# Optimization experiments

Hardware: AMD Instinct MI355X
Metric: run time of the kernel (lower is better)

## Reference

```python
import jax, jax.numpy as jnp
import numpy as np

D_MODEL = 512
PROJ = 2 * D_MODEL  # 1024
N_STATES = 32
KSIZE = 4
LN_EPS = 1e-3  # keras LayerNormalization default epsilon


def setup_inputs() -> dict:
    key = jax.random.key(0)
    ks = jax.random.split(key, 16)
    B, L = 2, 2048
    s_in = 1.0 / np.sqrt(D_MODEL)
    s_pr = 1.0 / np.sqrt(PROJ)
    x = jax.random.normal(ks[0], (B, L, D_MODEL), dtype=jnp.float32)
    # LayerNorm params
    ln_gamma = jnp.ones((D_MODEL,), jnp.float32)
    ln_beta = jnp.zeros((D_MODEL,), jnp.float32)
    # dense1 / dense2: d_model -> proj
    W1 = jax.random.normal(ks[1], (D_MODEL, PROJ), jnp.float32) * s_in
    b1 = jnp.zeros((PROJ,), jnp.float32)
    W2 = jax.random.normal(ks[2], (D_MODEL, PROJ), jnp.float32) * s_in
    b2 = jnp.zeros((PROJ,), jnp.float32)
    # depthwise causal conv1d: kernel (K, 1, PROJ) in WIO layout, groups=PROJ
    conv_k = jax.random.normal(ks[3], (KSIZE, 1, PROJ), jnp.float32) * 0.5
    conv_b = jnp.zeros((PROJ,), jnp.float32)
    # SSM params
    A_log = jnp.log(jnp.broadcast_to(jnp.arange(1, N_STATES + 1, dtype=jnp.float32), (PROJ, N_STATES)))
    D_skip = jnp.ones((PROJ,), jnp.float32)
    WB = jax.random.normal(ks[4], (PROJ, N_STATES), jnp.float32) * s_pr
    bB = jnp.zeros((N_STATES,), jnp.float32)
    WC = jax.random.normal(ks[5], (PROJ, N_STATES), jnp.float32) * s_pr
    bC = jnp.zeros((N_STATES,), jnp.float32)
    Wd = jax.random.normal(ks[6], (PROJ, PROJ), jnp.float32) * s_pr
    bd = jnp.zeros((PROJ,), jnp.float32)
    # dense3: proj -> d_model
    W3 = jax.random.normal(ks[7], (PROJ, D_MODEL), jnp.float32) * s_pr
    b3 = jnp.zeros((D_MODEL,), jnp.float32)
    return dict(x=x, ln_gamma=ln_gamma, ln_beta=ln_beta, W1=W1, b1=b1, W2=W2, b2=b2,
                conv_k=conv_k, conv_b=conv_b, A_log=A_log, D_skip=D_skip,
                WB=WB, bB=bB, WC=WC, bC=bC, Wd=Wd, bd=bd, W3=W3, b3=b3)


def _layernorm(x, gamma, beta):
    mu = jnp.mean(x, axis=-1, keepdims=True)
    var = jnp.mean(jnp.square(x - mu), axis=-1, keepdims=True)
    return (x - mu) * jax.lax.rsqrt(var + LN_EPS) * gamma + beta


def _causal_dwconv(x, k, b):
    # x: [B,L,C], k: [K,1,C], depthwise causal conv (left-pad K-1)
    y = jax.lax.conv_general_dilated(
        x, k, window_strides=(1,), padding=[(KSIZE - 1, 0)],
        dimension_numbers=('NWC', 'WIO', 'NWC'), feature_group_count=PROJ)
    return y + b


def _selective_scan(u, delta, A, Bm, Cm, D_skip):
    # u, delta: [B,L,D]; A: [D,N]; Bm, Cm: [B,L,N]; D_skip: [D]
    deltaA = jnp.einsum('bld,dn->bldn', delta, A)                 # [B,L,D,N]
    deltaBu = jnp.einsum('bld,bld,bln->bldn', delta, u, Bm)        # [B,L,D,N]
    # shift deltaA left by one along L, zero at the end (pad trick in source)
    shifted = jnp.concatenate([deltaA[:, 1:], jnp.zeros_like(deltaA[:, :1])], axis=1)
    # reversed cumsum along L, then exp
    e = jnp.exp(jnp.flip(jnp.cumsum(jnp.flip(shifted, axis=1), axis=1), axis=1))
    xs = jnp.cumsum(deltaBu * e, axis=1) / (e + 1e-12)
    y = jnp.einsum('bldn,bln->bld', xs, Cm)
    return y + u * D_skip


def reference(x, ln_gamma, ln_beta, W1, b1, W2, b2, conv_k, conv_b,
              A_log, D_skip, WB, bB, WC, bC, Wd, bd, W3, b3):
    h = _layernorm(x, ln_gamma, ln_beta)
    x1 = h @ W1 + b1                      # [B,L,PROJ]
    x1 = _causal_dwconv(x1, conv_k, conv_b)
    x1 = jax.nn.silu(x1)
    A = -jnp.exp(A_log)                    # [PROJ,N]
    Cm = x1 @ WC + bC                      # [B,L,N]
    Bm = x1 @ WB + bB                      # [B,L,N]
    delta = jax.nn.softplus(x1 @ Wd + bd)  # [B,L,PROJ]
    y = _selective_scan(x1, delta, A, Bm, Cm, D_skip)
    x2 = jax.nn.silu(h @ W2 + b2)
    out = (y * x2) @ W3 + b3 + x           # residual; dropout is identity at inference
    return out
```

## Files before the change

kernel.cpp:

```cpp
#include <hip/hip_runtime.h>
#include <stdint.h>

#define L_SEQ 2048
#define BATCH 2
#define DMODEL 512
#define PROJ 1024
#define NST 32
#define NCATU 1088
#define ROWS (BATCH*L_SEQ)
#define THRESH 50.0f

typedef float f32x4 __attribute__((ext_vector_type(4)));
typedef short short8 __attribute__((ext_vector_type(8)));

__device__ inline float bf2f(unsigned short u){ uint32_t x=((uint32_t)u)<<16; float f; __builtin_memcpy(&f,&x,4); return f; }
__device__ inline unsigned short f2bf(float f){ uint32_t x; __builtin_memcpy(&x,&f,4); uint32_t r=x+0x7FFFu+((x>>16)&1u); return (unsigned short)(r>>16); }
__device__ inline float siluf(float x){ return x/(1.f+__expf(-x)); }
__device__ inline float softplusf(float x){ return x>20.f? x : log1pf(__expf(x)); }

#define AS1(p) ((const __attribute__((address_space(1))) void*)(p))
#define AS3(p) ((__attribute__((address_space(3))) void*)(p))

template<int N> __device__ inline void wait_vmcnt(){
  if constexpr (N==0)      asm volatile("s_waitcnt vmcnt(0)" ::: "memory");
  else if constexpr (N==4) asm volatile("s_waitcnt vmcnt(4)" ::: "memory");
  else if constexpr (N==8) asm volatile("s_waitcnt vmcnt(8)" ::: "memory");
  else                     asm volatile("s_waitcnt vmcnt(12)" ::: "memory");
}

__global__ __launch_bounds__(256)
void prep_ln_kernel(const float* __restrict__ W1, const float* __restrict__ b1,
                    const float* __restrict__ W2, const float* __restrict__ b2,
                    const float* __restrict__ Wd, const float* __restrict__ bd,
                    const float* __restrict__ WB, const float* __restrict__ bB,
                    const float* __restrict__ WC, const float* __restrict__ bC,
                    const float* __restrict__ W3,
                    unsigned short* __restrict__ W12t, unsigned short* __restrict__ Wcatt,
                    unsigned short* __restrict__ W3t, float* __restrict__ bias12,
                    float* __restrict__ biascat,
                    const float* __restrict__ x, const float* __restrict__ ln_g,
                    const float* __restrict__ ln_b, unsigned short* __restrict__ H)
{
  __shared__ float tile[32][33];
  int bid = blockIdx.x;
  int lx = threadIdx.x & 31, ly = threadIdx.x >> 5;
  if (bid < 1024) {
    int kt = bid & 15, nt = bid >> 4;
    int k0 = kt*32, n0 = nt*32;
    const float* S = (n0 < 1024) ? W1 : W2;
    int nc = (n0 < 1024) ? n0 : n0 - 1024;
#pragma unroll
    for (int i=0;i<4;i++)
      tile[ly+i*8][lx] = S[(size_t)(k0+ly+i*8)*1024 + nc + lx];
    __syncthreads();
#pragma unroll
    for (int i=0;i<4;i++)
      W12t[(size_t)(n0+ly+i*8)*512 + k0 + lx] = f2bf(tile[lx][ly+i*8]);
    return;
  }
  if (bid < 2112) {
    int t = bid - 1024;
    int kt = t & 31, nt = t >> 5;
    int k0 = kt*32, n0 = nt*32;
#pragma unroll
    for (int i=0;i<4;i++){
      int k = k0 + ly + i*8;
      float v;
      if (n0 < 1024)       v = Wd[(size_t)k*1024 + n0 + lx];
      else if (n0 == 1024) v = WB[(size_t)k*32 + lx];
      else                 v = WC[(size_t)k*32 + lx];
      tile[ly+i*8][lx] = v;
    }
    __syncthreads();
#pragma unroll
    for (int i=0;i<4;i++)
      Wcatt[(size_t)(n0+ly+i*8)*1024 + k0 + lx] = f2bf(tile[lx][ly+i*8]);
    return;
  }
  if (bid < 2624) {
    int t = bid - 2112;
    int kt = t & 31, nt = t >> 5;
    int k0 = kt*32, n0 = nt*32;
#pragma unroll
    for (int i=0;i<4;i++)
      tile[ly+i*8][lx] = W3[(size_t)(k0+ly+i*8)*512 + n0 + lx];
    __syncthreads();
#pragma unroll
    for (int i=0;i<4;i++)
      W3t[(size_t)(n0+ly+i*8)*1024 + k0 + lx] = f2bf(tile[lx][ly+i*8]);
    return;
  }
  if (bid < 2637) {
    int j = (bid - 2624)*256 + threadIdx.x;
    if (j < 2048) { bias12[j] = (j < 1024) ? b1[j] : b2[j-1024]; return; }
    j -= 2048;
    if (j < NCATU) biascat[j] = (j < 1024) ? bd[j] : (j < 1056) ? bB[j-1024] : bC[j-1056];
    return;
  }
  int row = (bid - 2637)*4 + (threadIdx.x >> 6);
  int lane = threadIdx.x & 63;
  const float4* xr = (const float4*)(x + (size_t)row*DMODEL);
  float4 v0 = xr[lane];
  float4 v1 = xr[lane+64];
  float s = v0.x+v0.y+v0.z+v0.w + v1.x+v1.y+v1.z+v1.w;
  float q = v0.x*v0.x+v0.y*v0.y+v0.z*v0.z+v0.w*v0.w
          + v1.x*v1.x+v1.y*v1.y+v1.z*v1.z+v1.w*v1.w;
#pragma unroll
  for (int m=32;m>0;m>>=1){ s += __shfl_xor(s,m); q += __shfl_xor(q,m); }
  float mu = s*(1.f/DMODEL);
  float var = q*(1.f/DMODEL) - mu*mu;
  float rs = rsqrtf(var + 1e-3f);
  int c0 = lane*4, c1 = 256 + lane*4;
  float4 g0 = *(const float4*)&ln_g[c0]; float4 g1 = *(const float4*)&ln_g[c1];
  float4 t0 = *(const float4*)&ln_b[c0]; float4 t1 = *(const float4*)&ln_b[c1];
  ushort4 o0, o1;
  o0.x = f2bf((v0.x-mu)*rs*g0.x + t0.x);
  o0.y = f2bf((v0.y-mu)*rs*g0.y + t0.y);
  o0.z = f2bf((v0.z-mu)*rs*g0.z + t0.z);
  o0.w = f2bf((v0.w-mu)*rs*g0.w + t0.w);
  o1.x = f2bf((v1.x-mu)*rs*g1.x + t1.x);
  o1.y = f2bf((v1.y-mu)*rs*g1.y + t1.y);
  o1.z = f2bf((v1.z-mu)*rs*g1.z + t1.z);
  o1.w = f2bf((v1.w-mu)*rs*g1.w + t1.w);
  *(ushort4*)&H[(size_t)row*DMODEL + c0] = o0;
  *(ushort4*)&H[(size_t)row*DMODEL + c1] = o1;
}

template<int MODE>
__global__ __launch_bounds__(256)
void gemm64(const unsigned short* __restrict__ A, const unsigned short* __restrict__ Bt,
            void* __restrict__ Cv, void* __restrict__ Cv2, const float* __restrict__ bias,
            int M, int N, int K, int Kfull)
{
  constexpr int BK = 64;
  constexpr int LPT = 4;
  __shared__ unsigned short As[3][64*BK];
  __shared__ unsigned short Bs[3][64*BK];
  int tid = threadIdx.x;
  int lane = tid & 63, wid = tid >> 6;
  int wm = wid >> 1, wn = wid & 1;
  int gx = gridDim.x;
  int nwg = gx * gridDim.y;
  int L = blockIdx.y*gx + blockIdx.x;
  int W = (L & 7)*(nwg >> 3) + (L >> 3);
  int bx = W % gx, by = W / gx;
  int m0 = bx*64, n0 = by*64;
  int kofs = blockIdx.z*K;

  f32x4 acc[2][2];
#pragma unroll
  for (int i=0;i<2;i++)
#pragma unroll
    for (int j=0;j<2;j++)
#pragma unroll
      for (int e=0;e<4;e++) acc[i][j][e] = 0.f;

  const unsigned short* ap[2];
  const unsigned short* bp[2];
#pragma unroll
  for (int j=0;j<2;j++){
    int s = tid + j*256;
    int row = s >> 3, kc = ((s & 7) ^ (row & 7)) * 8;
    ap[j] = A + (size_t)(m0+row)*Kfull + kofs + kc;
    bp[j] = Bt + (size_t)(n0+row)*Kfull + kofs + kc;
  }
  auto stage = [&](int buf){
#pragma unroll
    for (int j=0;j<2;j++){
      __builtin_amdgcn_global_load_lds(AS1(ap[j]), AS3(&As[buf][(size_t)(j*256 + wid*64)*8]), 16, 0, 0);
      ap[j] += BK;
    }
#pragma unroll
    for (int j=0;j<2;j++){
      __builtin_amdgcn_global_load_lds(AS1(bp[j]), AS3(&Bs[buf][(size_t)(j*256 + wid*64)*8]), 16, 0, 0);
      bp[j] += BK;
    }
  };
  stage(0); stage(1);
  int T = K/BK;
  int rb = 0, wb = 2;
  int r = lane & 15, kb = lane >> 4;
  for (int t = 0; t < T; ++t) {
    if (t+1 < T) wait_vmcnt<LPT>();
    else         wait_vmcnt<0>();
    __builtin_amdgcn_s_barrier();
    if (t+2 < T) { stage(wb); wb = (wb==2)?0:wb+1; }
#pragma unroll
    for (int ks=0; ks<2; ++ks) {
      int cx = (ks*4 + kb) ^ (r & 7);
      short8 af[2], bfr[2];
#pragma unroll
      for (int i=0;i<2;i++) af[i]  = *(const short8*)&As[rb][((wm*32 + i*16 + r)*8 + cx)*8];
#pragma unroll
      for (int j=0;j<2;j++) bfr[j] = *(const short8*)&Bs[rb][((wn*32 + j*16 + r)*8 + cx)*8];
      __builtin_amdgcn_s_setprio(1);
#pragma unroll
      for (int i=0;i<2;i++)
#pragma unroll
        for (int j=0;j<2;j++)
          acc[i][j] = __builtin_amdgcn_mfma_f32_16x16x32_bf16(af[i], bfr[j], acc[i][j], 0,0,0);
      __builtin_amdgcn_s_setprio(0);
    }
    rb = (rb==2)?0:rb+1;
  }
  int rr = (lane >> 4)*4, cc = lane & 15;
#pragma unroll
  for (int i=0;i<2;i++)
#pragma unroll
    for (int j=0;j<2;j++) {
      int col = n0 + wn*32 + j*16 + cc;
#pragma unroll
      for (int e=0;e<4;e++) {
        int row = m0 + wm*32 + i*16 + rr + e;
        float v = acc[i][j][e];
        if constexpr (MODE == 1) {
          v += bias[col];
          if (col < 1024) ((unsigned short*)Cv)[(size_t)row*1024 + col] = f2bf(v);
          else            ((unsigned short*)Cv2)[(size_t)row*1024 + col - 1024] = f2bf(siluf(v));
        } else if constexpr (MODE == 2) {
          v += bias[row];
          if (row < 1024) v = softplusf(v);
          ((float*)Cv)[(size_t)row*N + col] = v;
        } else {
          ((float*)Cv)[(size_t)blockIdx.z*M*N + (size_t)row*N + col] = v;
        }
      }
    }
}

__global__ __launch_bounds__(256)
void reduce_kernel(const float* __restrict__ P, const float* __restrict__ x,
                   const float* __restrict__ b3, float* __restrict__ out)
{
  size_t i = ((size_t)blockIdx.x*256 + threadIdx.x)*4;
  int col = (int)(i & 511);
  float4 a = *(const float4*)&P[i];
  float4 b = *(const float4*)&P[(size_t)ROWS*512 + i];
  float4 xv = *(const float4*)&x[i];
  float4 bv = *(const float4*)&b3[col];
  float4 o;
  o.x = a.x + b.x + xv.x + bv.x;
  o.y = a.y + b.y + xv.y + bv.y;
  o.z = a.z + b.z + xv.z + bv.z;
  o.w = a.w + b.w + xv.w + bv.w;
  *(float4*)&out[i] = o;
}

__global__ __launch_bounds__(256)
void conv_silu_kernel(const unsigned short* __restrict__ P12n, const float* __restrict__ ck,
                      const float* __restrict__ cb, unsigned short* __restrict__ ubf)
{
  int gid = blockIdx.x*256 + threadIdx.x;
  int c = (gid & 255)*4;
  int row = gid >> 8;
  int l = row & (L_SEQ-1);
  float4 bv = *(const float4*)&cb[c];
  float r0=bv.x, r1=bv.y, r2=bv.z, r3=bv.w;
#pragma unroll
  for (int t=0;t<4;t++){
    int lsrc = l - 3 + t;
    if (lsrc >= 0) {
      ushort4 xv = *(const ushort4*)&P12n[(size_t)(row-3+t)*1024 + c];
      float4 kv = *(const float4*)&ck[t*PROJ + c];
      r0 = fmaf(bf2f(xv.x),kv.x,r0);
      r1 = fmaf(bf2f(xv.y),kv.y,r1);
      r2 = fmaf(bf2f(xv.z),kv.z,r2);
      r3 = fmaf(bf2f(xv.w),kv.w,r3);
    }
  }
  ushort4 o;
  o.x=f2bf(siluf(r0)); o.y=f2bf(siluf(r1)); o.z=f2bf(siluf(r2)); o.w=f2bf(siluf(r3));
  *(ushort4*)&ubf[(size_t)row*PROJ + c] = o;
}

__global__ __launch_bounds__(256)
void zmul_pre_kernel(const unsigned short* __restrict__ ubf, const unsigned short* __restrict__ x2bf,
                     const float* __restrict__ Dskip, unsigned short* __restrict__ zbf)
{
  size_t i = ((size_t)blockIdx.x*256 + threadIdx.x)*4;
  int d = (int)(i & (PROJ-1));
  ushort4 uu = *(const ushort4*)&ubf[i];
  ushort4 xx = *(const ushort4*)&x2bf[i];
  float4 Dv = *(const float4*)&Dskip[d];
  ushort4 o;
  o.x = f2bf(bf2f(uu.x)*Dv.x*bf2f(xx.x));
  o.y = f2bf(bf2f(uu.y)*Dv.y*bf2f(xx.y));
  o.z = f2bf(bf2f(uu.z)*Dv.z*bf2f(xx.z));
  o.w = f2bf(bf2f(uu.w)*Dv.w*bf2f(xx.w));
  *(ushort4*)&zbf[i] = o;
}

__global__ __launch_bounds__(256)
void sscan_kernel(const float* __restrict__ CT, const unsigned short* __restrict__ ubf,
                  const unsigned short* __restrict__ x2bf, const float* __restrict__ Dskip,
                  const float* __restrict__ A_log, unsigned short* __restrict__ zbf)
{
  __shared__ float ps[256];
  __shared__ float suf8sh[256];
  __shared__ int   cs[256];
  __shared__ float Alds[8][32];
  __shared__ float Slds[8][32];
  __shared__ int baseSh;
  int tid = threadIdx.x;
  int G = blockIdx.x;
  int b = G >> 10, d = G & 1023;
  const float* dT = CT + (size_t)d*ROWS + b*L_SEQ;

  float4 a0 = *(const float4*)&dT[tid*8];
  float4 a1 = *(const float4*)&dT[tid*8+4];
  float vals[8] = {a0.x,a0.y,a0.z,a0.w,a1.x,a1.y,a1.z,a1.w};
  float part = 0.f;
#pragma unroll
  for (int i=0;i<8;i++) part += vals[i];
  ps[tid] = part; __syncthreads();
  for (int off=1; off<256; off<<=1){
    float v = (tid >= off) ? ps[tid-off] : 0.f;
    __syncthreads();
    ps[tid] += v;
    __syncthreads();
  }
  float Tot = ps[255];
  float prefx = ps[tid] - part;
  suf8sh[tid] = Tot - prefx;
  int cnt = 0; float run = prefx;
#pragma unroll
  for (int i=0;i<8;i++){ cnt += (Tot - run >= THRESH) ? 1 : 0; run += vals[i]; }
  cs[tid] = cnt; __syncthreads();
  for (int off=128; off>0; off>>=1){ if (tid < off) cs[tid] += cs[tid+off]; __syncthreads(); }
  if (tid == 0) {
    int total = cs[0];
    int l0 = total > 0 ? total-1 : 0;
    baseSh = l0 & ~7;
  }
  __syncthreads();
  int base = baseSh;

  int n = tid & 31, seg = tid >> 5;
  int segStart = seg*256, segEnd = segStart + 256;
  float np1 = __expf(A_log[d*NST + n]);
  float Ds = Dskip[d];
  const float* Br = CT + (size_t)(1024+n)*ROWS + b*L_SEQ;
  const float* Cr = CT + (size_t)(1056+n)*ROWS + b*L_SEQ;
  const unsigned short* ub = ubf + (size_t)b*L_SEQ*PROJ + d;
  const unsigned short* xb = x2bf + (size_t)b*L_SEQ*PROJ + d;
  unsigned short* zb = zbf + (size_t)b*L_SEQ*PROJ + d;

  bool active = segEnd > base;
  int sFirst = base >> 8;
  int lstart = max(segStart, base);

  if (active && seg < 7) {
    float s = 0.f, Ap = 1.f;
    for (int l = lstart; l < segEnd; l += 8) {
      float4 d0 = *(const float4*)&dT[l];
      float4 d1 = *(const float4*)&dT[l+4];
      float4 B0 = *(const float4*)&Br[l];
      float4 B1 = *(const float4*)&Br[l+4];
      float uu[8];
#pragma unroll
      for (int t=0;t<8;t++) uu[t] = bf2f(ub[(size_t)(l+t)*PROJ]);
      float dl[8] = {d0.x,d0.y,d0.z,d0.w,d1.x,d1.y,d1.z,d1.w};
      float Bv[8] = {B0.x,B0.y,B0.z,B0.w,B1.x,B1.y,B1.z,B1.w};
#pragma unroll
      for (int t=0;t<8;t++){
        float decay = __expf(-dl[t]*np1);
        s = fmaf(decay, s, dl[t]*uu[t]*Bv[t]);
        Ap *= decay;
      }
    }
    Alds[seg][n] = Ap; Slds[seg][n] = s;
  }
  __syncthreads();

  float sin = 0.f;
  if (active) {
    for (int c = sFirst; c < seg; ++c)
      sin = fmaf(Alds[c][n], sin, Slds[c][n]);
  }

  if (active) {
    float s = sin;
    for (int l = lstart; l < segEnd; l += 8) {
      float4 d0 = *(const float4*)&dT[l];
      float4 d1 = *(const float4*)&dT[l+4];
      float4 B0 = *(const float4*)&Br[l];
      float4 B1 = *(const float4*)&Br[l+4];
      float4 C0 = *(const float4*)&Cr[l];
      float4 C1 = *(const float4*)&Cr[l+4];
      float uu[8], xx[8];
#pragma unroll
      for (int t=0;t<8;t++) uu[t] = bf2f(ub[(size_t)(l+t)*PROJ]);
#pragma unroll
      for (int t=0;t<8;t++) xx[t] = bf2f(xb[(size_t)(l+t)*PROJ]);
      float sufv = suf8sh[l >> 3];
      float dl[8] = {d0.x,d0.y,d0.z,d0.w,d1.x,d1.y,d1.z,d1.w};
      float Bv[8] = {B0.x,B0.y,B0.z,B0.w,B1.x,B1.y,B1.z,B1.w};
      float Cv[8] = {C0.x,C0.y,C0.z,C0.w,C1.x,C1.y,C1.z,C1.w};
      float cum = 0.f;
#pragma unroll
      for (int t=0;t<8;t++){
        cum += dl[t];
        float decay = __expf(-dl[t]*np1);
        s = fmaf(decay, s, dl[t]*uu[t]*Bv[t]);
        float gte = 1.f/(1.f + 1e-12f*__expf(np1*(sufv - cum)));
        float contrib = s*gte*Cv[t];
#pragma unroll
        for (int m=16;m>0;m>>=1) contrib += __shfl_xor(contrib, m);
        if (n == 0)
          zb[(size_t)(l+t)*PROJ] = f2bf((contrib + uu[t]*Ds)*xx[t]);
      }
    }
  }
}

extern "C" void kernel_launch(void* const* d_in, const int* in_sizes, int n_in,
                              void* d_out, int out_size, void* d_ws, size_t ws_size,
                              hipStream_t stream)
{
  const float* x     = (const float*)d_in[0];
  const float* ln_g  = (const float*)d_in[1];
  const float* ln_b  = (const float*)d_in[2];
  const float* W1    = (const float*)d_in[3];
  const float* b1    = (const float*)d_in[4];
  const float* W2    = (const float*)d_in[5];
  const float* b2    = (const float*)d_in[6];
  const float* convk = (const float*)d_in[7];
  const float* convb = (const float*)d_in[8];
  const float* A_log = (const float*)d_in[9];
  const float* Dskip = (const float*)d_in[10];
  const float* WB    = (const float*)d_in[11];
  const float* bB    = (const float*)d_in[12];
  const float* WC    = (const float*)d_in[13];
  const float* bC    = (const float*)d_in[14];
  const float* Wd    = (const float*)d_in[15];
  const float* bd    = (const float*)d_in[16];
  const float* W3    = (const float*)d_in[17];
  const float* b3    = (const float*)d_in[18];

  char* w = (char*)d_ws;
  auto alloc = [&](size_t bytes){ char* p = w; w += (bytes + 255) & ~(size_t)255; return p; };
  unsigned short* Hbf    = (unsigned short*)alloc((size_t)ROWS*DMODEL*2);
  unsigned short* W12t   = (unsigned short*)alloc((size_t)2048*512*2);
  unsigned short* Wcatt  = (unsigned short*)alloc((size_t)NCATU*1024*2);
  unsigned short* W3t    = (unsigned short*)alloc((size_t)512*1024*2);
  float*          bias12 = (float*)alloc(2048*4);
  float*          biascat= (float*)alloc(NCATU*4);
  unsigned short* P12n   = (unsigned short*)alloc((size_t)ROWS*1024*2);
  unsigned short* ubf    = (unsigned short*)alloc((size_t)ROWS*PROJ*2);
  unsigned short* x2bf   = (unsigned short*)alloc((size_t)ROWS*PROJ*2);
  float*          CT     = (float*)alloc((size_t)NCATU*ROWS*4);
  unsigned short* zbf    = (unsigned short*)alloc((size_t)ROWS*PROJ*2);
  float*          Pp     = (float*)alloc((size_t)2*ROWS*512*4);

  prep_ln_kernel<<<3661, 256, 0, stream>>>(W1,b1,W2,b2,Wd,bd,WB,bB,WC,bC,W3,
                                           W12t,Wcatt,W3t,bias12,biascat,
                                           x, ln_g, ln_b, Hbf);

  dim3 g1(ROWS/64, 2048/64);
  gemm64<1><<<g1, 256, 0, stream>>>(Hbf, W12t, P12n, x2bf, bias12, ROWS, 2048, DMODEL, DMODEL);

  conv_silu_kernel<<<ROWS*256/256, 256, 0, stream>>>(P12n, convk, convb, ubf);

  zmul_pre_kernel<<<(ROWS*PROJ/4)/256, 256, 0, stream>>>(ubf, x2bf, Dskip, zbf);

  dim3 g2(NCATU/64, ROWS/64);
  gemm64<2><<<g2, 256, 0, stream>>>(Wcatt, ubf, CT, nullptr, biascat, NCATU, ROWS, PROJ, PROJ);

  sscan_kernel<<<2048, 256, 0, stream>>>(CT, ubf, x2bf, Dskip, A_log, zbf);

  dim3 g3(ROWS/64, 512/64, 2);
  gemm64<5><<<g3, 256, 0, stream>>>(zbf, W3t, Pp, nullptr, b3, ROWS, 512, 512, PROJ);
  reduce_kernel<<<(ROWS*512/4)/256, 256, 0, stream>>>(Pp, x, b3, (float*)d_out);
}
```

Baseline: 153.9 us.

## Transpose u and x2 to channel-major and software-pipeline scan loads

Adds a tiled shared-memory transpose kernel that writes u and x2 in channel-major (d, row) layout. The selective-scan kernel can then read them with contiguous ushort4 vector loads instead of strided scalar loads spaced 2 KB apart. Both scan loops are also restructured to prefetch the next 8-step chunk of delta, B, C, u and x2 while the current one is computed. The cost is an extra kernel launch, two 8 MB extra buffers and additional global traffic for the transpose.

```diff
diff --git a/kernel.cpp b/kernel.cpp
--- a/kernel.cpp
+++ b/kernel.cpp
@@ -274,6 +274,24 @@
 }
 
 __global__ __launch_bounds__(256)
+void utrans_kernel(const unsigned short* __restrict__ u, const unsigned short* __restrict__ x2,
+                   unsigned short* __restrict__ uT, unsigned short* __restrict__ x2T)
+{
+  __shared__ unsigned short tile[32][33];
+  const unsigned short* src = blockIdx.z ? x2 : u;
+  unsigned short* dst = blockIdx.z ? x2T : uT;
+  int r0 = blockIdx.x*32, c0 = blockIdx.y*32;
+  int lx = threadIdx.x & 31, ly = threadIdx.x >> 5;
+#pragma unroll
+  for (int i=0;i<4;i++)
+    tile[ly+i*8][lx] = src[(size_t)(r0+ly+i*8)*1024 + c0 + lx];
+  __syncthreads();
+#pragma unroll
+  for (int i=0;i<4;i++)
+    dst[(size_t)(c0+ly+i*8)*ROWS + r0 + lx] = tile[lx][ly+i*8];
+}
+
+__global__ __launch_bounds__(256)
 void zmul_pre_kernel(const unsigned short* __restrict__ ubf, const unsigned short* __restrict__ x2bf,
                      const float* __restrict__ Dskip, unsigned short* __restrict__ zbf)
 {
@@ -291,8 +309,8 @@
 }
 
 __global__ __launch_bounds__(256)
-void sscan_kernel(const float* __restrict__ CT, const unsigned short* __restrict__ ubf,
-                  const unsigned short* __restrict__ x2bf, const float* __restrict__ Dskip,
+void sscan_kernel(const float* __restrict__ CT, const unsigned short* __restrict__ uT,
+                  const unsigned short* __restrict__ x2T, const float* __restrict__ Dskip,
                   const float* __restrict__ A_log, unsigned short* __restrict__ zbf)
 {
   __shared__ float ps[256];
@@ -341,8 +359,8 @@
   float Ds = Dskip[d];
   const float* Br = CT + (size_t)(1024+n)*ROWS + b*L_SEQ;
   const float* Cr = CT + (size_t)(1056+n)*ROWS + b*L_SEQ;
-  const unsigned short* ub = ubf + (size_t)b*L_SEQ*PROJ + d;
-  const unsigned short* xb = x2bf + (size_t)b*L_SEQ*PROJ + d;
+  const unsigned short* ub = uT  + (size_t)d*ROWS + b*L_SEQ;
+  const unsigned short* xb = x2T + (size_t)d*ROWS + b*L_SEQ;
   unsigned short* zb = zbf + (size_t)b*L_SEQ*PROJ + d;
 
   bool active = segEnd > base;
@@ -351,22 +369,30 @@
 
   if (active && seg < 7) {
     float s = 0.f, Ap = 1.f;
-    for (int l = lstart; l < segEnd; l += 8) {
-      float4 d0 = *(const float4*)&dT[l];
-      float4 d1 = *(const float4*)&dT[l+4];
-      float4 B0 = *(const float4*)&Br[l];
-      float4 B1 = *(const float4*)&Br[l+4];
-      float uu[8];
-#pragma unroll
-      for (int t=0;t<8;t++) uu[t] = bf2f(ub[(size_t)(l+t)*PROJ]);
+    int l = lstart;
+    float4 d0=*(const float4*)&dT[l], d1=*(const float4*)&dT[l+4];
+    float4 B0=*(const float4*)&Br[l], B1=*(const float4*)&Br[l+4];
+    ushort4 u0=*(const ushort4*)&ub[l], u1=*(const ushort4*)&ub[l+4];
+    while (l < segEnd) {
+      int ln = l + 8;
+      float4 nd0,nd1,nB0,nB1; ushort4 nu0,nu1;
+      if (ln < segEnd) {
+        nd0=*(const float4*)&dT[ln]; nd1=*(const float4*)&dT[ln+4];
+        nB0=*(const float4*)&Br[ln]; nB1=*(const float4*)&Br[ln+4];
+        nu0=*(const ushort4*)&ub[ln]; nu1=*(const ushort4*)&ub[ln+4];
+      }
       float dl[8] = {d0.x,d0.y,d0.z,d0.w,d1.x,d1.y,d1.z,d1.w};
       float Bv[8] = {B0.x,B0.y,B0.z,B0.w,B1.x,B1.y,B1.z,B1.w};
+      float uu[8] = {bf2f(u0.x),bf2f(u0.y),bf2f(u0.z),bf2f(u0.w),
+                     bf2f(u1.x),bf2f(u1.y),bf2f(u1.z),bf2f(u1.w)};
 #pragma unroll
       for (int t=0;t<8;t++){
         float decay = __expf(-dl[t]*np1);
         s = fmaf(decay, s, dl[t]*uu[t]*Bv[t]);
         Ap *= decay;
       }
+      l = ln;
+      d0=nd0; d1=nd1; B0=nB0; B1=nB1; u0=nu0; u1=nu1;
     }
     Alds[seg][n] = Ap; Slds[seg][n] = s;
   }
@@ -380,22 +406,30 @@
 
   if (active) {
     float s = sin;
-    for (int l = lstart; l < segEnd; l += 8) {
-      float4 d0 = *(const float4*)&dT[l];
-      float4 d1 = *(const float4*)&dT[l+4];
-      float4 B0 = *(const float4*)&Br[l];
-      float4 B1 = *(const float4*)&Br[l+4];
-      float4 C0 = *(const float4*)&Cr[l];
-      float4 C1 = *(const float4*)&Cr[l+4];
-      float uu[8], xx[8];
-#pragma unroll
-      for (int t=0;t<8;t++) uu[t] = bf2f(ub[(size_t)(l+t)*PROJ]);
-#pragma unroll
-      for (int t=0;t<8;t++) xx[t] = bf2f(xb[(size_t)(l+t)*PROJ]);
+    int l = lstart;
+    float4 d0=*(const float4*)&dT[l], d1=*(const float4*)&dT[l+4];
+    float4 B0=*(const float4*)&Br[l], B1=*(const float4*)&Br[l+4];
+    float4 C0=*(const float4*)&Cr[l], C1=*(const float4*)&Cr[l+4];
+    ushort4 u0=*(const ushort4*)&ub[l], u1=*(const ushort4*)&ub[l+4];
+    ushort4 x0=*(const ushort4*)&xb[l], x1=*(const ushort4*)&xb[l+4];
+    while (l < segEnd) {
+      int ln = l + 8;
+      float4 nd0,nd1,nB0,nB1,nC0,nC1; ushort4 nu0,nu1,nx0,nx1;
+      if (ln < segEnd) {
+        nd0=*(const float4*)&dT[ln]; nd1=*(const float4*)&dT[ln+4];
+        nB0=*(const float4*)&Br[ln]; nB1=*(const float4*)&Br[ln+4];
+        nC0=*(const float4*)&Cr[ln]; nC1=*(const float4*)&Cr[ln+4];
+        nu0=*(const ushort4*)&ub[ln]; nu1=*(const ushort4*)&ub[ln+4];
+        nx0=*(const ushort4*)&xb[ln]; nx1=*(const ushort4*)&xb[ln+4];
+      }
       float sufv = suf8sh[l >> 3];
       float dl[8] = {d0.x,d0.y,d0.z,d0.w,d1.x,d1.y,d1.z,d1.w};
       float Bv[8] = {B0.x,B0.y,B0.z,B0.w,B1.x,B1.y,B1.z,B1.w};
       float Cv[8] = {C0.x,C0.y,C0.z,C0.w,C1.x,C1.y,C1.z,C1.w};
+      float uu[8] = {bf2f(u0.x),bf2f(u0.y),bf2f(u0.z),bf2f(u0.w),
+                     bf2f(u1.x),bf2f(u1.y),bf2f(u1.z),bf2f(u1.w)};
+      float xx[8] = {bf2f(x0.x),bf2f(x0.y),bf2f(x0.z),bf2f(x0.w),
+                     bf2f(x1.x),bf2f(x1.y),bf2f(x1.z),bf2f(x1.w)};
       float cum = 0.f;
 #pragma unroll
       for (int t=0;t<8;t++){
@@ -409,6 +443,9 @@
         if (n == 0)
           zb[(size_t)(l+t)*PROJ] = f2bf((contrib + uu[t]*Ds)*xx[t]);
       }
+      l = ln;
+      d0=nd0; d1=nd1; B0=nB0; B1=nB1; C0=nC0; C1=nC1;
+      u0=nu0; u1=nu1; x0=nx0; x1=nx1;
     }
   }
 }
@@ -448,6 +485,8 @@
   unsigned short* P12n   = (unsigned short*)alloc((size_t)ROWS*1024*2);
   unsigned short* ubf    = (unsigned short*)alloc((size_t)ROWS*PROJ*2);
   unsigned short* x2bf   = (unsigned short*)alloc((size_t)ROWS*PROJ*2);
+  unsigned short* uT     = (unsigned short*)alloc((size_t)PROJ*ROWS*2);
+  unsigned short* x2T    = (unsigned short*)alloc((size_t)PROJ*ROWS*2);
   float*          CT     = (float*)alloc((size_t)NCATU*ROWS*4);
   unsigned short* zbf    = (unsigned short*)alloc((size_t)ROWS*PROJ*2);
   float*          Pp     = (float*)alloc((size_t)2*ROWS*512*4);
@@ -461,12 +500,15 @@
 
   conv_silu_kernel<<<ROWS*256/256, 256, 0, stream>>>(P12n, convk, convb, ubf);
 
+  dim3 gt(ROWS/32, PROJ/32, 2);
+  utrans_kernel<<<gt, 256, 0, stream>>>(ubf, x2bf, uT, x2T);
+
   zmul_pre_kernel<<<(ROWS*PROJ/4)/256, 256, 0, stream>>>(ubf, x2bf, Dskip, zbf);
 
   dim3 g2(NCATU/64, ROWS/64);
   gemm64<2><<<g2, 256, 0, stream>>>(Wcatt, ubf, CT, nullptr, biascat, NCATU, ROWS, PROJ, PROJ);
 
-  sscan_kernel<<<2048, 256, 0, stream>>>(CT, ubf, x2bf, Dskip, A_log, zbf);
+  sscan_kernel<<<2048, 256, 0, stream>>>(CT, uT, x2T, Dskip, A_log, zbf);
 
   dim3 g3(ROWS/64, 512/64, 2);
   gemm64<5><<<g3, 256, 0, stream>>>(zbf, W3t, Pp, nullptr, b3, ROWS, 512, 512, PROJ);
```

Measured after the change: 159.7 us. 3.8% more time.
